# Kernel optimization log

Measured on AMD Instinct MI355X. Metric: run time of the kernel, lower is better.

The kernel has to match this reference:

```python
import jax, jax.numpy as jnp
import numpy as np

B, L = 2048, 8192
IN, H, OUT = 128, 512, 10
N_FRAMES = L // IN  # frame_step == frame_size -> non-overlapping unfold == reshape


def _lstm_layer(xs, W_ih, W_hh, b):
    """xs: [T, B, D_in]; returns (hs [T, B, H], h_T [B, H]).
    PyTorch gate order: i, f, g, o."""
    Bsz = xs.shape[1]
    h0 = jnp.zeros((Bsz, H), xs.dtype)
    c0 = jnp.zeros((Bsz, H), xs.dtype)

    def step(carry, x_t):
        h, c = carry
        gates = x_t @ W_ih.T + h @ W_hh.T + b  # [B, 4H]
        i, f, g, o = jnp.split(gates, 4, axis=-1)
        c = jax.nn.sigmoid(f) * c + jax.nn.sigmoid(i) * jnp.tanh(g)
        h = jax.nn.sigmoid(o) * jnp.tanh(c)
        return (h, c), h

    (hT, _), hs = jax.lax.scan(step, (h0, c0), xs)
    return hs, hT


def setup_inputs() -> dict:
    key = jax.random.key(0)
    ks = jax.random.split(key, 12)
    s_in = 1.0 / np.sqrt(H)
    return {
        "xb": jax.random.normal(ks[0], (B, L), jnp.float32),
        "W_ih0": jax.random.normal(ks[1], (4 * H, IN), jnp.float32) * s_in,
        "W_hh0": jax.random.normal(ks[2], (4 * H, H), jnp.float32) * s_in,
        "b0": jax.random.normal(ks[3], (4 * H,), jnp.float32) * s_in,
        "W_ih1": jax.random.normal(ks[4], (4 * H, H), jnp.float32) * s_in,
        "W_hh1": jax.random.normal(ks[5], (4 * H, H), jnp.float32) * s_in,
        "b1": jax.random.normal(ks[6], (4 * H,), jnp.float32) * s_in,
        "W_out": jax.random.normal(ks[7], (OUT, H), jnp.float32) * s_in,
        "b_out": jax.random.normal(ks[8], (OUT,), jnp.float32) * s_in,
    }


def reference(xb, W_ih0, W_hh0, b0, W_ih1, W_hh1, b1, W_out, b_out):
    # unfold(1, fs, fs) with step==size -> reshape; transpose to time-major
    frames = xb.reshape(B, N_FRAMES, IN).transpose(1, 0, 2)  # [T, B, IN]
    hs0, _ = _lstm_layer(frames, W_ih0, W_hh0, b0)           # [T, B, H]
    _, hT1 = _lstm_layer(hs0, W_ih1, W_hh1, b1)              # [B, H]
    return hT1 @ W_out.T + b_out                             # [B, OUT]
```

## Files before the change

kernel.cpp:

```cpp
#include <hip/hip_runtime.h>
#include <hip/hip_bf16.h>


typedef _Float16 f16x8 __attribute__((ext_vector_type(8)));
typedef float f32x4 __attribute__((ext_vector_type(4)));

#define Bsz 2048
#define Lsz 8192
#define Tsz 64

__global__ void cvt_f32_f16(const float* __restrict__ src, _Float16* __restrict__ dst, int n4) {
    int stride = gridDim.x * blockDim.x;
    for (int i = blockIdx.x * blockDim.x + threadIdx.x; i < n4; i += stride) {
        float4 v = ((const float4*)src)[i];
        union { _Float16 h[4]; ushort4 u; } o;
        o.h[0] = (_Float16)v.x; o.h[1] = (_Float16)v.y;
        o.h[2] = (_Float16)v.z; o.h[3] = (_Float16)v.w;
        ((ushort4*)dst)[i] = o.u;
    }
}

__global__ void pack_w(const float* __restrict__ Wih, const float* __restrict__ Whh,
                       _Float16* __restrict__ dst, int K1) {
    int KT = K1 + 512;
    int n4 = 2048 * KT / 4;
    int stride = gridDim.x * blockDim.x;
    for (int i = blockIdx.x * blockDim.x + threadIdx.x; i < n4; i += stride) {
        int row = i / (KT / 4);
        int col = (i % (KT / 4)) * 4;
        const float* s = (col < K1) ? (Wih + (size_t)row * K1 + col)
                                    : (Whh + (size_t)row * 512 + (col - K1));
        float4 v = *(const float4*)s;
        union { _Float16 h[4]; ushort4 u; } o;
        o.h[0] = (_Float16)v.x; o.h[1] = (_Float16)v.y;
        o.h[2] = (_Float16)v.z; o.h[3] = (_Float16)v.w;
        ((ushort4*)dst)[i] = o.u;
    }
}

__device__ __forceinline__ float fsig(float x)  { return 1.0f / (1.0f + __expf(-x)); }
__device__ __forceinline__ float ftanh(float x) { return 1.0f - 2.0f / (__expf(2.0f * x) + 1.0f); }

template<int K1>
__device__ __forceinline__ void stage_tiles(
    const _Float16* __restrict__ A1, int lda1,
    const _Float16* __restrict__ A2,
    const _Float16* __restrict__ Wcat,
    int grpc, int rowblk, int k0, char* dst, int tid)
{
    constexpr int KT = K1 + 512;
    const int wv = tid >> 6;
#pragma unroll
    for (int q = 0; q < 8; ++q) {
        const int j  = q * 64 + (tid >> 3);
        const int cg = (((tid & 7) ^ (j & 7)) << 3);
        const int wrow = ((j >> 7) << 9) + grpc * 128 + (j & 127);
        const _Float16* src = Wcat + (size_t)wrow * KT + k0 + cg;
        __builtin_amdgcn_global_load_lds(
            (const __attribute__((address_space(1))) void*)src,
            (__attribute__((address_space(3))) void*)(dst + q * 8192 + wv * 1024),
            16, 0, 0);
    }
    {
        const int row  = tid >> 3;
        const int cg   = (((tid & 7) ^ (row & 7)) << 3);
        const int kcol = k0 + cg;
        const int brow = rowblk * 64 + row;
        const _Float16* src = (kcol < K1)
            ? (A1 + (size_t)brow * lda1 + kcol)
            : (A2 + (size_t)brow * 512 + (kcol - K1));
        __builtin_amdgcn_global_load_lds(
            (const __attribute__((address_space(1))) void*)src,
            (__attribute__((address_space(3))) void*)(dst + 65536 + wv * 1024),
            16, 0, 0);
    }
}

template<int K1>
__device__ __forceinline__ void step_tile_v5(
    const _Float16* __restrict__ A1, int lda1,
    const _Float16* __restrict__ A2,
    const _Float16* __restrict__ Wcat,
    const float* __restrict__ bias,
    float* __restrict__ c,
    _Float16* __restrict__ h_out,
    int rowblk, int grpc, char* lds)
{
    constexpr int KT  = K1 + 512;
    constexpr int NIT = KT / 64;
    const int tid = threadIdx.x;
    const int ln  = tid & 63;
    const int wc  = tid >> 6;
    const int llo = ln & 15, lhi = ln >> 4;

    f32x4 acc[4][4] = {};

    stage_tiles<K1>(A1, lda1, A2, Wcat, grpc, rowblk, 0, lds, tid);
    __syncthreads();

    for (int it = 0; it < NIT; ++it) {
        char* cur = lds + (it & 1) * 73728;
        if (it + 1 < NIT)
            stage_tiles<K1>(A1, lda1, A2, Wcat, grpc, rowblk, (it + 1) * 64,
                            lds + ((it + 1) & 1) * 73728, tid);
#pragma unroll
        for (int ks = 0; ks < 2; ++ks) {
            const int gsw = (((ks * 4 + lhi) ^ (llo & 7)) << 4);
            f16x8 a[4], b[4];
#pragma unroll
            for (int mi = 0; mi < 4; ++mi)
                a[mi] = *(const f16x8*)(cur + 65536 + (mi * 16 + llo) * 128 + gsw);
#pragma unroll
            for (int cf = 0; cf < 4; ++cf)
                b[cf] = *(const f16x8*)(cur + (wc * 64 + cf * 16 + llo) * 128 + gsw);
#pragma unroll
            for (int mi = 0; mi < 4; ++mi)
#pragma unroll
                for (int cf = 0; cf < 4; ++cf)
                    acc[mi][cf] = __builtin_amdgcn_mfma_f32_16x16x32_f16(
                        a[mi], b[cf], acc[mi][cf], 0, 0, 0);
        }
        __syncthreads();
    }

    float* gl = (float*)lds;
#pragma unroll
    for (int mi = 0; mi < 4; ++mi)
#pragma unroll
        for (int cf = 0; cf < 4; ++cf) {
            const int col = wc * 64 + cf * 16 + llo;
#pragma unroll
            for (int r = 0; r < 4; ++r) {
                const int row = mi * 16 + lhi * 4 + r;
                gl[row * 512 + col] = acc[mi][cf][r];
            }
        }
    __syncthreads();

    const int lc   = tid & 127;
    const int r0   = tid >> 7;
    const int hcol = grpc * 128 + lc;
    float bz[4];
#pragma unroll
    for (int g = 0; g < 4; ++g) bz[g] = bias[g * 512 + hcol];
#pragma unroll
    for (int i = 0; i < 16; ++i) {
        const int row = i * 4 + r0;
        float iv = gl[row * 512 +   0 + lc] + bz[0];
        float fv = gl[row * 512 + 128 + lc] + bz[1];
        float gv = gl[row * 512 + 256 + lc] + bz[2];
        float ov = gl[row * 512 + 384 + lc] + bz[3];
        const size_t idx = (size_t)(rowblk * 64 + row) * 512 + hcol;
        float co = c[idx];
        float cn = fsig(fv) * co + fsig(iv) * ftanh(gv);
        float hn = fsig(ov) * ftanh(cn);
        c[idx] = cn;
        h_out[idx] = (_Float16)hn;
    }
}

__global__ __launch_bounds__(512, 2) void lstm_round(
    int t0, int t1,
    const _Float16* __restrict__ xb16,
    const _Float16* __restrict__ Wc0, const float* __restrict__ b0, float* __restrict__ c0,
    _Float16* __restrict__ h00, _Float16* __restrict__ h01,
    const _Float16* __restrict__ Wc1, const float* __restrict__ b1, float* __restrict__ c1,
    _Float16* __restrict__ h10, _Float16* __restrict__ h11)
{
    __shared__ __align__(16) char lds[147456];
    const int bid    = blockIdx.x;
    const int grp    = bid & 7;
    const int rowblk = bid >> 3;

    if (grp < 4) {
        if (t0 < 0) return;
        const _Float16* hr = (t0 & 1) ? h01 : h00;
        _Float16*       hw = (t0 & 1) ? h00 : h01;
        step_tile_v5<128>(xb16 + (size_t)t0 * 128, Lsz, hr, Wc0, b0, c0, hw, rowblk, grp, lds);
    } else {
        if (t1 < 0) return;
        const _Float16* h0in = ((t1 + 1) & 1) ? h01 : h00;
        const _Float16* hr   = (t1 & 1) ? h11 : h10;
        _Float16*       hw   = (t1 & 1) ? h10 : h11;
        step_tile_v5<512>(h0in, 512, hr, Wc1, b1, c1, hw, rowblk, grp - 4, lds);
    }
}

__global__ void proj_kernel(const _Float16* __restrict__ h1,
                            const float* __restrict__ Wout,
                            const float* __restrict__ bout,
                            float* __restrict__ out)
{
    int tid = blockIdx.x * blockDim.x + threadIdx.x;
    if (tid >= Bsz * 10) return;
    int b = tid / 10, o = tid % 10;
    float s = bout[o];
    const _Float16* hrow = h1 + (size_t)b * 512;
    const float* wrow = Wout + (size_t)o * 512;
    for (int k = 0; k < 512; ++k) s += (float)hrow[k] * wrow[k];
    out[tid] = s;
}

extern "C" void kernel_launch(void* const* d_in, const int* in_sizes, int n_in,
                              void* d_out, int out_size, void* d_ws, size_t ws_size,
                              hipStream_t stream) {
    const float* xb    = (const float*)d_in[0];
    const float* W_ih0 = (const float*)d_in[1];
    const float* W_hh0 = (const float*)d_in[2];
    const float* b0    = (const float*)d_in[3];
    const float* W_ih1 = (const float*)d_in[4];
    const float* W_hh1 = (const float*)d_in[5];
    const float* b1    = (const float*)d_in[6];
    const float* W_out = (const float*)d_in[7];
    const float* b_out = (const float*)d_in[8];
    float* out = (float*)d_out;

    char* ws = (char*)d_ws;
    size_t off = 0;
    auto alloc = [&](size_t bytes) -> void* {
        void* p = ws + off;
        off += (bytes + 255) & ~(size_t)255;
        return p;
    };
    _Float16* xb16 = (_Float16*)alloc((size_t)Bsz * Lsz * 2);
    _Float16* Wc0  = (_Float16*)alloc((size_t)2048 * 640 * 2);
    _Float16* Wc1  = (_Float16*)alloc((size_t)2048 * 1024 * 2);
    _Float16* h00  = (_Float16*)alloc((size_t)Bsz * 512 * 2);
    _Float16* h01  = (_Float16*)alloc((size_t)Bsz * 512 * 2);
    _Float16* h10  = (_Float16*)alloc((size_t)Bsz * 512 * 2);
    _Float16* h11  = (_Float16*)alloc((size_t)Bsz * 512 * 2);
    float* c0 = (float*)alloc((size_t)Bsz * 512 * 4);
    float* c1 = (float*)alloc((size_t)Bsz * 512 * 4);

    cvt_f32_f16<<<2048, 256, 0, stream>>>(xb, xb16, Bsz * Lsz / 4);
    pack_w<<<1280, 256, 0, stream>>>(W_ih0, W_hh0, Wc0, 128);
    pack_w<<<2048, 256, 0, stream>>>(W_ih1, W_hh1, Wc1, 512);

    hipMemsetAsync(h00, 0, (size_t)Bsz * 512 * 2, stream);
    hipMemsetAsync(h10, 0, (size_t)Bsz * 512 * 2, stream);
    hipMemsetAsync(c0, 0, (size_t)Bsz * 512 * 4, stream);
    hipMemsetAsync(c1, 0, (size_t)Bsz * 512 * 4, stream);

    for (int r = 0; r <= Tsz; ++r) {
        int t0 = (r < Tsz) ? r : -1;
        int t1 = r - 1;
        lstm_round<<<dim3(256), 512, 0, stream>>>(t0, t1,
            xb16, Wc0, b0, c0, h00, h01,
            Wc1, b1, c1, h10, h11);
    }

    proj_kernel<<<(Bsz * 10 + 255) / 256, 256, 0, stream>>>(h10, W_out, b_out, out);
}
```

Measured before the change: 1.756 ms.

## Retile LSTM step to 256 batch rows by 32 hidden columns per block

```diff
diff --git a/kernel.cpp b/kernel.cpp
--- a/kernel.cpp
+++ b/kernel.cpp
@@ -42,74 +42,76 @@
 __device__ __forceinline__ float ftanh(float x) { return 1.0f - 2.0f / (__expf(2.0f * x) + 1.0f); }
 
 template<int K1>
-__device__ __forceinline__ void stage_tiles(
+__device__ __forceinline__ void stage_v6(
     const _Float16* __restrict__ A1, int lda1,
     const _Float16* __restrict__ A2,
     const _Float16* __restrict__ Wcat,
-    int grpc, int rowblk, int k0, char* dst, int tid)
+    int hcb, int rowtile, int k0, char* buf, int tid)
 {
     constexpr int KT = K1 + 512;
     const int wv = tid >> 6;
 #pragma unroll
-    for (int q = 0; q < 8; ++q) {
+    for (int q = 0; q < 2; ++q) {
         const int j  = q * 64 + (tid >> 3);
         const int cg = (((tid & 7) ^ (j & 7)) << 3);
-        const int wrow = ((j >> 7) << 9) + grpc * 128 + (j & 127);
+        const int wrow = ((j >> 5) << 9) + hcb * 32 + (j & 31);
         const _Float16* src = Wcat + (size_t)wrow * KT + k0 + cg;
         __builtin_amdgcn_global_load_lds(
             (const __attribute__((address_space(1))) void*)src,
-            (__attribute__((address_space(3))) void*)(dst + q * 8192 + wv * 1024),
+            (__attribute__((address_space(3))) void*)(buf + q * 8192 + wv * 1024),
             16, 0, 0);
     }
-    {
-        const int row  = tid >> 3;
+#pragma unroll
+    for (int q = 0; q < 4; ++q) {
+        const int row  = q * 64 + (tid >> 3);
         const int cg   = (((tid & 7) ^ (row & 7)) << 3);
         const int kcol = k0 + cg;
-        const int brow = rowblk * 64 + row;
+        const int brow = rowtile * 256 + row;
         const _Float16* src = (kcol < K1)
             ? (A1 + (size_t)brow * lda1 + kcol)
             : (A2 + (size_t)brow * 512 + (kcol - K1));
         __builtin_amdgcn_global_load_lds(
             (const __attribute__((address_space(1))) void*)src,
-            (__attribute__((address_space(3))) void*)(dst + 65536 + wv * 1024),
+            (__attribute__((address_space(3))) void*)(buf + 16384 + q * 8192 + wv * 1024),
             16, 0, 0);
     }
 }
 
 template<int K1>
-__device__ __forceinline__ void step_tile_v5(
+__device__ __forceinline__ void step_v6(
     const _Float16* __restrict__ A1, int lda1,
     const _Float16* __restrict__ A2,
     const _Float16* __restrict__ Wcat,
     const float* __restrict__ bias,
     float* __restrict__ c,
     _Float16* __restrict__ h_out,
-    int rowblk, int grpc, char* lds)
+    int rowtile, int hcb, char* lds)
 {
     constexpr int KT  = K1 + 512;
     constexpr int NIT = KT / 64;
     const int tid = threadIdx.x;
     const int ln  = tid & 63;
-    const int wc  = tid >> 6;
+    const int wv  = tid >> 6;
     const int llo = ln & 15, lhi = ln >> 4;
+    const int wr  = wv >> 1, wc = wv & 1;
 
     f32x4 acc[4][4] = {};
 
-    stage_tiles<K1>(A1, lda1, A2, Wcat, grpc, rowblk, 0, lds, tid);
+    stage_v6<K1>(A1, lda1, A2, Wcat, hcb, rowtile, 0, lds, tid);
     __syncthreads();
 
     for (int it = 0; it < NIT; ++it) {
-        char* cur = lds + (it & 1) * 73728;
+        char* cur = lds + (it & 1) * 49152;
         if (it + 1 < NIT)
-            stage_tiles<K1>(A1, lda1, A2, Wcat, grpc, rowblk, (it + 1) * 64,
-                            lds + ((it + 1) & 1) * 73728, tid);
+            stage_v6<K1>(A1, lda1, A2, Wcat, hcb, rowtile, (it + 1) * 64,
+                         lds + ((it + 1) & 1) * 49152, tid);
 #pragma unroll
         for (int ks = 0; ks < 2; ++ks) {
             const int gsw = (((ks * 4 + lhi) ^ (llo & 7)) << 4);
             f16x8 a[4], b[4];
 #pragma unroll
             for (int mi = 0; mi < 4; ++mi)
-                a[mi] = *(const f16x8*)(cur + 65536 + (mi * 16 + llo) * 128 + gsw);
+                a[mi] = *(const f16x8*)(cur + 16384 + (wr * 64 + mi * 16 + llo) * 128 + gsw);
 #pragma unroll
             for (int cf = 0; cf < 4; ++cf)
                 b[cf] = *(const f16x8*)(cur + (wc * 64 + cf * 16 + llo) * 128 + gsw);
@@ -131,26 +133,26 @@
             const int col = wc * 64 + cf * 16 + llo;
 #pragma unroll
             for (int r = 0; r < 4; ++r) {
-                const int row = mi * 16 + lhi * 4 + r;
-                gl[row * 512 + col] = acc[mi][cf][r];
+                const int row = wr * 64 + mi * 16 + lhi * 4 + r;
+                gl[row * 128 + col] = acc[mi][cf][r];
             }
         }
     __syncthreads();
 
-    const int lc   = tid & 127;
-    const int r0   = tid >> 7;
-    const int hcol = grpc * 128 + lc;
+    const int lc   = tid & 31;
+    const int ro   = tid >> 5;
+    const int hcol = hcb * 32 + lc;
     float bz[4];
 #pragma unroll
     for (int g = 0; g < 4; ++g) bz[g] = bias[g * 512 + hcol];
 #pragma unroll
     for (int i = 0; i < 16; ++i) {
-        const int row = i * 4 + r0;
-        float iv = gl[row * 512 +   0 + lc] + bz[0];
-        float fv = gl[row * 512 + 128 + lc] + bz[1];
-        float gv = gl[row * 512 + 256 + lc] + bz[2];
-        float ov = gl[row * 512 + 384 + lc] + bz[3];
-        const size_t idx = (size_t)(rowblk * 64 + row) * 512 + hcol;
+        const int row = i * 16 + ro;
+        float iv = gl[row * 128 +  0 + lc] + bz[0];
+        float fv = gl[row * 128 + 32 + lc] + bz[1];
+        float gv = gl[row * 128 + 64 + lc] + bz[2];
+        float ov = gl[row * 128 + 96 + lc] + bz[3];
+        const size_t idx = (size_t)(rowtile * 256 + row) * 512 + hcol;
         float co = c[idx];
         float cn = fsig(fv) * co + fsig(iv) * ftanh(gv);
         float hn = fsig(ov) * ftanh(cn);
@@ -167,22 +169,25 @@
     const _Float16* __restrict__ Wc1, const float* __restrict__ b1, float* __restrict__ c1,
     _Float16* __restrict__ h10, _Float16* __restrict__ h11)
 {
-    __shared__ __align__(16) char lds[147456];
-    const int bid    = blockIdx.x;
-    const int grp    = bid & 7;
-    const int rowblk = bid >> 3;
-
-    if (grp < 4) {
+    __shared__ __align__(16) char lds[131072];
+    const int bid     = blockIdx.x;
+    const int x       = bid & 7;
+    const int q       = bid >> 3;
+    const int layer   = q >> 4;
+    const int rowtile = (q >> 1) & 7;
+    const int hcb     = x * 2 + (q & 1);
+
+    if (layer == 0) {
         if (t0 < 0) return;
         const _Float16* hr = (t0 & 1) ? h01 : h00;
         _Float16*       hw = (t0 & 1) ? h00 : h01;
-        step_tile_v5<128>(xb16 + (size_t)t0 * 128, Lsz, hr, Wc0, b0, c0, hw, rowblk, grp, lds);
+        step_v6<128>(xb16 + (size_t)t0 * 128, Lsz, hr, Wc0, b0, c0, hw, rowtile, hcb, lds);
     } else {
         if (t1 < 0) return;
         const _Float16* h0in = ((t1 + 1) & 1) ? h01 : h00;
         const _Float16* hr   = (t1 & 1) ? h11 : h10;
         _Float16*       hw   = (t1 & 1) ? h10 : h11;
-        step_tile_v5<512>(h0in, 512, hr, Wc1, b1, c1, hw, rowblk, grp - 4, lds);
+        step_v6<512>(h0in, 512, hr, Wc1, b1, c1, hw, rowtile, hcb, lds);
     }
 }
 
```

Result: faster. 1.668 ms (-5.1%).
